# Optimization experiments

Measured on AMD Instinct MI355X. Metric: run time of the kernel, lower is better.

The kernel has to match this reference:

```python
import jax, jax.numpy as jnp
import numpy as np

NUM_HEADS = 8
DIM_HEAD = 128
SCALE = DIM_HEAD ** -0.5


def setup_inputs() -> dict:
    key = jax.random.key(0)
    ks = jax.random.split(key, 6)
    B, N, D = 8, 1024, 1024
    return {
        "s_v": jax.random.normal(ks[0], (B, N, D), jnp.float32),
        "s_m": jax.random.normal(ks[1], (B, N, D), jnp.float32),
        "g_l": jax.random.normal(ks[2], (B, NUM_HEADS, N, N), jnp.float32),
        "W_qkv": jax.random.normal(ks[3], (D, 3 * NUM_HEADS * DIM_HEAD), jnp.float32) * (D ** -0.5),
        "W_qk": jax.random.normal(ks[4], (D, 2 * NUM_HEADS * DIM_HEAD), jnp.float32) * (D ** -0.5),
        "W_out": jax.random.normal(ks[5], (NUM_HEADS * DIM_HEAD, D), jnp.float32) * ((NUM_HEADS * DIM_HEAD) ** -0.5),
        "b_out": jnp.zeros((D,), jnp.float32),
    }


def _split_heads(t):
    # [b, n, h*d] -> [b, h, n, d]
    b, n, hd = t.shape
    return t.reshape(b, n, NUM_HEADS, DIM_HEAD).transpose(0, 2, 1, 3)


def reference(s_v, s_m, g_l, W_qkv, W_qk, W_out, b_out):
    b, n, _ = s_v.shape
    q_v, k_v, v = [_split_heads(t) for t in jnp.split(s_v @ W_qkv, 3, axis=-1)]
    q_m, k_m = [_split_heads(t) for t in jnp.split(s_m @ W_qk, 2, axis=-1)]
    # trajectory attention probs (softmaxed) times raw value-stream scores
    p_m = jax.nn.softmax(jnp.einsum('bhid,bhjd->bhij', q_m, k_m), axis=-1)
    p_v = jnp.einsum('bhid,bhjd->bhij', q_v, k_v)
    dots = p_m * p_v * SCALE + g_l
    attn = jax.nn.softmax(dots, axis=-1)
    out = jnp.einsum('bhij,bhjd->bhid', attn, v)
    out = out.transpose(0, 2, 1, 3).reshape(b, n, NUM_HEADS * DIM_HEAD)
    return out @ W_out + b_out
```

## Files before the change

kernel.cpp:

```cpp
#include <hip/hip_runtime.h>

typedef __attribute__((ext_vector_type(8))) short short8;
typedef __attribute__((ext_vector_type(8))) unsigned short ushortx8;
typedef __attribute__((ext_vector_type(4))) unsigned short ushortx4;
typedef __attribute__((ext_vector_type(4))) float floatx4;

#define SCALE_F 0.08838834764831845f

__device__ __forceinline__ float b2f(unsigned short u) {
  union { unsigned int u; float f; } c; c.u = ((unsigned int)u) << 16; return c.f;
}
__device__ __forceinline__ unsigned short f2b(float f) {
  union { float f; unsigned int u; } c; c.f = f;
  unsigned int u = c.u;
  u += 0x7fffu + ((u >> 16) & 1u);
  return (unsigned short)(u >> 16);
}

#define GLD_LDS16(g, l)                                              \
  __builtin_amdgcn_global_load_lds(                                  \
      (const __attribute__((address_space(1))) void*)(g),            \
      (__attribute__((address_space(3))) void*)(l), 16, 0, 0)

__global__ __launch_bounds__(256) void cast_bf16_kernel(
    const float* __restrict__ x, unsigned short* __restrict__ y, int n) {
  int i = (blockIdx.x * 256 + threadIdx.x) * 4;
  if (i >= n) return;
  float4 v = *(const float4*)(x + i);
  ushortx4 o;
  o[0] = f2b(v.x); o[1] = f2b(v.y); o[2] = f2b(v.z); o[3] = f2b(v.w);
  *(ushortx4*)(y + i) = o;
}

__global__ __launch_bounds__(256) void split2_kernel(
    const float* __restrict__ x, unsigned short* __restrict__ y) {
  int idx = blockIdx.x * 256 + threadIdx.x;
  int row = idx >> 8;
  int c4 = (idx & 255) * 4;
  float4 v = *(const float4*)(x + (size_t)row * 1024 + c4);
  ushortx4 hi, lo;
  hi[0] = f2b(v.x); lo[0] = f2b(v.x - b2f(hi[0]));
  hi[1] = f2b(v.y); lo[1] = f2b(v.y - b2f(hi[1]));
  hi[2] = f2b(v.z); lo[2] = f2b(v.z - b2f(hi[2]));
  hi[3] = f2b(v.w); lo[3] = f2b(v.w - b2f(hi[3]));
  unsigned short* yr = y + (size_t)row * 2048;
  *(ushortx4*)(yr + c4) = hi;
  *(ushortx4*)(yr + 1024 + c4) = lo;
}

__global__ __launch_bounds__(256) void transpose_split_qk(
    const float* __restrict__ W, unsigned short* __restrict__ y) {
  __shared__ float tile[32][33];
  int t = threadIdx.x, tx = t & 31, ty = t >> 5;
  int n0 = blockIdx.x * 32, k0 = blockIdx.y * 32;
  for (int rr = ty; rr < 32; rr += 8)
    tile[rr][tx] = W[(size_t)(k0 + rr) * 2048 + n0 + tx];
  __syncthreads();
  for (int rr = ty; rr < 32; rr += 8) {
    float v = tile[tx][rr];
    unsigned short hi = f2b(v);
    unsigned short* yr = y + (size_t)(n0 + rr) * 2048;
    yr[k0 + tx] = hi;
    yr[1024 + k0 + tx] = hi;
  }
}

template<int MODE>
__global__ __launch_bounds__(256) void transpose_any(
    const void* __restrict__ inv, void* __restrict__ outv,
    int R, int C, int ldin, int ldout,
    long sIb, long sIh, long sOb, long sOh, int pstart) {
  int z = blockIdx.z, p = pstart + z, b = p >> 3, h = p & 7;
  size_t ioff = (size_t)(sIb * b + sIh * h);
  size_t ooff = (size_t)(sOb * b + sOh * h);
  __shared__ float tile[32][33];
  int t = threadIdx.x, tx = t & 31, ty = t >> 5;
  int c0 = blockIdx.x * 32, r0 = blockIdx.y * 32;
  for (int rr = ty; rr < 32; rr += 8) {
    size_t idx = ioff + (size_t)(r0 + rr) * ldin + (c0 + tx);
    tile[rr][tx] = (MODE == 2) ? b2f(((const unsigned short*)inv)[idx])
                               : ((const float*)inv)[idx];
  }
  __syncthreads();
  for (int rr = ty; rr < 32; rr += 8) {
    size_t idx = ooff + (size_t)(c0 + rr) * ldout + (r0 + tx);
    ((unsigned short*)outv)[idx] = f2b(tile[tx][rr]);
  }
}

template<int OUT_BF16, int ADD_BIAS>
__global__ __launch_bounds__(256) void gemm128(
    const unsigned short* __restrict__ A, const unsigned short* __restrict__ BT,
    void* __restrict__ Cv, const float* __restrict__ bias,
    int K, int lda, int ldb, int ldc,
    long sAz, long sAb, long sAh, long sBz, long sBb, long sBh,
    long sCz, long sCb, long sCh, int pstart) {
  int z = blockIdx.z, p = pstart + z, bb = p >> 3, hh = p & 7;
  A  += (size_t)(sAz * z + sAb * bb + sAh * hh);
  BT += (size_t)(sBz * z + sBb * bb + sBh * hh);
  size_t coff = (size_t)(sCz * z + sCb * bb + sCh * hh);

  __shared__ unsigned short Al[128][32];
  __shared__ unsigned short Bl[128][32];
  int t = threadIdx.x;
  int m0 = blockIdx.y * 128, n0 = blockIdx.x * 128;
  int w = t >> 6, l = t & 63;
  int wm = (w >> 1) * 64, wn = (w & 1) * 64;
  int lrow = l & 15, lq = l >> 4;
  floatx4 acc[4][4] = {};

  int srow = t >> 2, scol = (t & 3) * 8;
  const unsigned short* ga = A + (size_t)(m0 + srow) * lda + scol;
  const unsigned short* gb = BT + (size_t)(n0 + srow) * ldb + scol;
  unsigned short* la = &Al[srow][scol];
  unsigned short* lb = &Bl[srow][scol];
  size_t lda64 = (size_t)64 * lda, ldb64 = (size_t)64 * ldb;

  for (int k0 = 0; k0 < K; k0 += 32) {
    GLD_LDS16(ga + k0, la);
    GLD_LDS16(ga + lda64 + k0, la + 64 * 32);
    GLD_LDS16(gb + k0, lb);
    GLD_LDS16(gb + ldb64 + k0, lb + 64 * 32);
    __syncthreads();
    short8 af[4], bf[4];
#pragma unroll
    for (int i = 0; i < 4; i++) af[i] = *(const short8*)&Al[wm + i * 16 + lrow][lq * 8];
#pragma unroll
    for (int j = 0; j < 4; j++) bf[j] = *(const short8*)&Bl[wn + j * 16 + lrow][lq * 8];
#pragma unroll
    for (int i = 0; i < 4; i++)
#pragma unroll
      for (int j = 0; j < 4; j++)
        acc[i][j] = __builtin_amdgcn_mfma_f32_16x16x32_bf16(af[i], bf[j], acc[i][j], 0, 0, 0);
    __syncthreads();
  }
#pragma unroll
  for (int i = 0; i < 4; i++)
#pragma unroll
    for (int j = 0; j < 4; j++)
#pragma unroll
      for (int r = 0; r < 4; r++) {
        int row = m0 + wm + i * 16 + lq * 4 + r;
        int col = n0 + wn + j * 16 + lrow;
        float v = acc[i][j][r];
        if (ADD_BIAS) v += bias[col];
        size_t idx = coff + (size_t)row * ldc + col;
        if (OUT_BF16) ((unsigned short*)Cv)[idx] = f2b(v);
        else          ((float*)Cv)[idx] = v;
      }
}

template<int OUT_BF16, int ADD_BIAS>
__global__ __launch_bounds__(256) void gemm64(
    const unsigned short* __restrict__ A, const unsigned short* __restrict__ BT,
    void* __restrict__ Cv, const float* __restrict__ bias,
    int K, int lda, int ldb, int ldc,
    long sAz, long sAb, long sAh, long sBz, long sBb, long sBh,
    long sCz, long sCb, long sCh, int pstart) {
  int z = blockIdx.z, p = pstart + z, bb = p >> 3, hh = p & 7;
  A  += (size_t)(sAz * z + sAb * bb + sAh * hh);
  BT += (size_t)(sBz * z + sBb * bb + sBh * hh);
  size_t coff = (size_t)(sCz * z + sCb * bb + sCh * hh);

  __shared__ unsigned short Al[64][32];
  __shared__ unsigned short Bl[128][32];
  int t = threadIdx.x;
  int m0 = blockIdx.y * 64, n0 = blockIdx.x * 128;
  int w = t >> 6, l = t & 63;
  int wm = (w >> 1) * 32, wn = (w & 1) * 64;
  int lrow = l & 15, lq = l >> 4;
  floatx4 acc[2][4] = {};

  int srow = t >> 2, scol = (t & 3) * 8;
  const unsigned short* ga = A + (size_t)(m0 + srow) * lda + scol;
  const unsigned short* gb = BT + (size_t)(n0 + srow) * ldb + scol;
  unsigned short* la = &Al[srow][scol];
  unsigned short* lb = &Bl[srow][scol];
  size_t ldb64 = (size_t)64 * ldb;

  for (int k0 = 0; k0 < K; k0 += 32) {
    GLD_LDS16(ga + k0, la);
    GLD_LDS16(gb + k0, lb);
    GLD_LDS16(gb + ldb64 + k0, lb + 64 * 32);
    __syncthreads();
    short8 af[2], bf[4];
#pragma unroll
    for (int i = 0; i < 2; i++) af[i] = *(const short8*)&Al[wm + i * 16 + lrow][lq * 8];
#pragma unroll
    for (int j = 0; j < 4; j++) bf[j] = *(const short8*)&Bl[wn + j * 16 + lrow][lq * 8];
#pragma unroll
    for (int i = 0; i < 2; i++)
#pragma unroll
      for (int j = 0; j < 4; j++)
        acc[i][j] = __builtin_amdgcn_mfma_f32_16x16x32_bf16(af[i], bf[j], acc[i][j], 0, 0, 0);
    __syncthreads();
  }
#pragma unroll
  for (int i = 0; i < 2; i++)
#pragma unroll
    for (int j = 0; j < 4; j++)
#pragma unroll
      for (int r = 0; r < 4; r++) {
        int row = m0 + wm + i * 16 + lq * 4 + r;
        int col = n0 + wn + j * 16 + lrow;
        float v = acc[i][j][r];
        if (ADD_BIAS) v += bias[col];
        size_t idx = coff + (size_t)row * ldc + col;
        if (OUT_BF16) ((unsigned short*)Cv)[idx] = f2b(v);
        else          ((float*)Cv)[idx] = v;
      }
}

__global__ __launch_bounds__(256) void logits_prep(
    const float* __restrict__ qkf, unsigned short* __restrict__ qm,
    unsigned short* __restrict__ km, int pstart) {
  int idx = blockIdx.x * 256 + threadIdx.x;
  int z = blockIdx.y;
  int i = idx >> 5;
  int d4 = (idx & 31) * 4;
  int p = pstart + z, b = p >> 3, h = p & 7;
  const float* row = qkf + ((size_t)(b * 1024 + i)) * 2048 + h * 128;
  ushortx4 hi, lo;

  float4 q = *(const float4*)(row + d4);
  hi[0] = f2b(q.x); lo[0] = f2b(q.x - b2f(hi[0]));
  hi[1] = f2b(q.y); lo[1] = f2b(q.y - b2f(hi[1]));
  hi[2] = f2b(q.z); lo[2] = f2b(q.z - b2f(hi[2]));
  hi[3] = f2b(q.w); lo[3] = f2b(q.w - b2f(hi[3]));
  unsigned short* qr = qm + ((size_t)z * 1024 + i) * 384;
  *(ushortx4*)(qr + d4) = hi;
  *(ushortx4*)(qr + 128 + d4) = lo;
  *(ushortx4*)(qr + 256 + d4) = hi;

  float4 k = *(const float4*)(row + 1024 + d4);
  hi[0] = f2b(k.x); lo[0] = f2b(k.x - b2f(hi[0]));
  hi[1] = f2b(k.y); lo[1] = f2b(k.y - b2f(hi[1]));
  hi[2] = f2b(k.z); lo[2] = f2b(k.z - b2f(hi[2]));
  hi[3] = f2b(k.w); lo[3] = f2b(k.w - b2f(hi[3]));
  unsigned short* kr = km + ((size_t)z * 1024 + i) * 384;
  *(ushortx4*)(kr + d4) = hi;
  *(ushortx4*)(kr + 128 + d4) = hi;
  *(ushortx4*)(kr + 256 + d4) = lo;
}

__global__ __launch_bounds__(256) void softmax_combine(
    const float* __restrict__ smb, unsigned short* __restrict__ pvb,
    const float* __restrict__ g_l, int pstart) {
  int i = blockIdx.x, z = blockIdx.y;
  int p = pstart + z;
  const float* srow = smb + ((size_t)z * 1024 + i) * 1024;
  unsigned short* vrow = pvb + ((size_t)z * 1024 + i) * 1024;
  const float* grow = g_l + ((size_t)p * 1024 + i) * 1024;
  int t = threadIdx.x;
  __shared__ float red[4];

  float4 s = *(const float4*)(srow + t * 4);
  float mx = fmaxf(fmaxf(s.x, s.y), fmaxf(s.z, s.w));
#pragma unroll
  for (int o = 32; o; o >>= 1) mx = fmaxf(mx, __shfl_xor(mx, o));
  if ((t & 63) == 0) red[t >> 6] = mx;
  __syncthreads();
  mx = fmaxf(fmaxf(red[0], red[1]), fmaxf(red[2], red[3]));
  __syncthreads();
  float4 e;
  e.x = __expf(s.x - mx); e.y = __expf(s.y - mx);
  e.z = __expf(s.z - mx); e.w = __expf(s.w - mx);
  float sum = e.x + e.y + e.z + e.w;
#pragma unroll
  for (int o = 32; o; o >>= 1) sum += __shfl_xor(sum, o);
  if ((t & 63) == 0) red[t >> 6] = sum;
  __syncthreads();
  float inv = 1.0f / (red[0] + red[1] + red[2] + red[3]);
  __syncthreads();

  ushortx4 pv = *(const ushortx4*)(vrow + t * 4);
  float4 g = *(const float4*)(grow + t * 4);
  float4 d;
  d.x = e.x * inv * b2f(pv[0]) * SCALE_F + g.x;
  d.y = e.y * inv * b2f(pv[1]) * SCALE_F + g.y;
  d.z = e.z * inv * b2f(pv[2]) * SCALE_F + g.z;
  d.w = e.w * inv * b2f(pv[3]) * SCALE_F + g.w;

  float mx2 = fmaxf(fmaxf(d.x, d.y), fmaxf(d.z, d.w));
#pragma unroll
  for (int o = 32; o; o >>= 1) mx2 = fmaxf(mx2, __shfl_xor(mx2, o));
  if ((t & 63) == 0) red[t >> 6] = mx2;
  __syncthreads();
  mx2 = fmaxf(fmaxf(red[0], red[1]), fmaxf(red[2], red[3]));
  __syncthreads();
  float4 e2;
  e2.x = __expf(d.x - mx2); e2.y = __expf(d.y - mx2);
  e2.z = __expf(d.z - mx2); e2.w = __expf(d.w - mx2);
  float sum2 = e2.x + e2.y + e2.z + e2.w;
#pragma unroll
  for (int o = 32; o; o >>= 1) sum2 += __shfl_xor(sum2, o);
  if ((t & 63) == 0) red[t >> 6] = sum2;
  __syncthreads();
  float inv2 = 1.0f / (red[0] + red[1] + red[2] + red[3]);

  ushortx4 o4;
  o4[0] = f2b(e2.x * inv2); o4[1] = f2b(e2.y * inv2);
  o4[2] = f2b(e2.z * inv2); o4[3] = f2b(e2.w * inv2);
  *(ushortx4*)(vrow + t * 4) = o4;
}

extern "C" void kernel_launch(void* const* d_in, const int* in_sizes, int n_in,
                              void* d_out, int out_size, void* d_ws, size_t ws_size,
                              hipStream_t stream) {
  (void)in_sizes; (void)n_in; (void)out_size; (void)ws_size;
  const float* s_v   = (const float*)d_in[0];
  const float* s_m   = (const float*)d_in[1];
  const float* g_l   = (const float*)d_in[2];
  const float* W_qkv = (const float*)d_in[3];
  const float* W_qk  = (const float*)d_in[4];
  const float* W_out = (const float*)d_in[5];
  const float* b_out = (const float*)d_in[6];
  float* out = (float*)d_out;
  char* ws = (char*)d_ws;

  unsigned short* sv_bf  = (unsigned short*)(ws);
  unsigned short* qm384  = (unsigned short*)(ws);
  unsigned short* wtqkv  = (unsigned short*)(ws + 16777216);
  unsigned short* km384  = (unsigned short*)(ws + 16777216);
  unsigned short* wtout  = (unsigned short*)(ws + 29360128);
  unsigned short* qkvb   = (unsigned short*)(ws + 31457280);
  float*          qkf    = (float*)(ws + 81788928);
  unsigned short* vt     = (unsigned short*)(ws + 148897792);
  unsigned short* ao     = (unsigned short*)(ws + 165675008);
  unsigned short* smhl   = (unsigned short*)(ws + 182452224);
  float*          smb    = (float*)(ws + 182452224);
  unsigned short* wqk_hl = (unsigned short*)(ws + 249561088);
  unsigned short* pvb    = (unsigned short*)(ws + 249561088);

  cast_bf16_kernel<<<dim3(8192), 256, 0, stream>>>(s_v, sv_bf, 8388608);
  transpose_any<0><<<dim3(96, 32, 1), 256, 0, stream>>>(
      W_qkv, wtqkv, 1024, 3072, 3072, 1024, 0, 0, 0, 0, 0);
  transpose_any<0><<<dim3(32, 32, 1), 256, 0, stream>>>(
      W_out, wtout, 1024, 1024, 1024, 1024, 0, 0, 0, 0, 0);
  split2_kernel<<<dim3(8192), 256, 0, stream>>>(s_m, smhl);
  transpose_split_qk<<<dim3(64, 32, 1), 256, 0, stream>>>(W_qk, wqk_hl);
  gemm128<1, 0><<<dim3(24, 64, 1), 256, 0, stream>>>(
      sv_bf, wtqkv, qkvb, nullptr, 1024, 1024, 1024, 3072,
      0, 0, 0, 0, 0, 0, 0, 0, 0, 0);
  gemm128<0, 0><<<dim3(16, 64, 1), 256, 0, stream>>>(
      smhl, wqk_hl, qkf, nullptr, 2048, 2048, 2048, 2048,
      0, 0, 0, 0, 0, 0, 0, 0, 0, 0);
  transpose_any<2><<<dim3(4, 32, 64), 256, 0, stream>>>(
      qkvb + 2048, vt, 1024, 128, 3072, 1024,
      (long)1024 * 3072, 128, (long)1048576, 131072, 0);

  for (int c = 0; c < 4; c++) {
    int pstart = c * 16;
    logits_prep<<<dim3(128, 16), 256, 0, stream>>>(qkf, qm384, km384, pstart);
    gemm128<0, 0><<<dim3(8, 8, 16), 256, 0, stream>>>(
        qm384, km384, smb, nullptr, 384, 384, 384, 1024,
        (long)1024 * 384, 0, 0, (long)1024 * 384, 0, 0,
        (long)1048576, 0, 0, pstart);
    gemm128<1, 0><<<dim3(8, 8, 16), 256, 0, stream>>>(
        qkvb, qkvb + 1024, pvb, nullptr, 128, 3072, 3072, 1024,
        0, (long)1024 * 3072, 128, 0, (long)1024 * 3072, 128,
        (long)1048576, 0, 0, pstart);
    softmax_combine<<<dim3(1024, 16), 256, 0, stream>>>(smb, pvb, g_l, pstart);
    gemm64<1, 0><<<dim3(1, 16, 16), 256, 0, stream>>>(
        pvb, vt, ao, nullptr, 1024, 1024, 1024, 1024,
        (long)1048576, 0, 0, 0, (long)1048576, 131072,
        0, (long)1048576, 128, pstart);
  }
  gemm128<0, 1><<<dim3(8, 64, 1), 256, 0, stream>>>(
      ao, wtout, out, b_out, 1024, 1024, 1024, 1024,
      0, 0, 0, 0, 0, 0, 0, 0, 0, 0);
}
```

Measured before the change: 1.058 ms.

## Use wave-per-row softmax and single-pass batched attention when workspace allows

The softmax_combine kernel now gives each 64-lane wave one full row of 1024 elements. Reductions use only wave shuffles, with no shared memory or block barriers. When the workspace is large enough, a new memory layout holds all 64 batch-head slices at once, so the 4-chunk loop becomes one launch per stage, and the final attention-times-V GEMM switches from gemm64 to gemm128. This removes launch overhead and raises parallelism per launch, but needs a much larger workspace and falls back to the old chunked path if the workspace is too small.

```diff
diff --git a/kernel.cpp b/kernel.cpp
--- a/kernel.cpp
+++ b/kernel.cpp
@@ -246,68 +246,73 @@
 __global__ __launch_bounds__(256) void softmax_combine(
     const float* __restrict__ smb, unsigned short* __restrict__ pvb,
     const float* __restrict__ g_l, int pstart) {
-  int i = blockIdx.x, z = blockIdx.y;
-  int p = pstart + z;
+  int z = blockIdx.y, p = pstart + z;
+  int w = threadIdx.x >> 6, l = threadIdx.x & 63;
+  int i = blockIdx.x * 4 + w;
   const float* srow = smb + ((size_t)z * 1024 + i) * 1024;
   unsigned short* vrow = pvb + ((size_t)z * 1024 + i) * 1024;
   const float* grow = g_l + ((size_t)p * 1024 + i) * 1024;
-  int t = threadIdx.x;
-  __shared__ float red[4];
-
-  float4 s = *(const float4*)(srow + t * 4);
-  float mx = fmaxf(fmaxf(s.x, s.y), fmaxf(s.z, s.w));
+
+  float4 s[4];
+#pragma unroll
+  for (int j = 0; j < 4; j++) s[j] = *(const float4*)(srow + j * 256 + l * 4);
+  float mx = -3.0e38f;
+#pragma unroll
+  for (int j = 0; j < 4; j++)
+    mx = fmaxf(mx, fmaxf(fmaxf(s[j].x, s[j].y), fmaxf(s[j].z, s[j].w)));
 #pragma unroll
   for (int o = 32; o; o >>= 1) mx = fmaxf(mx, __shfl_xor(mx, o));
-  if ((t & 63) == 0) red[t >> 6] = mx;
-  __syncthreads();
-  mx = fmaxf(fmaxf(red[0], red[1]), fmaxf(red[2], red[3]));
-  __syncthreads();
-  float4 e;
-  e.x = __expf(s.x - mx); e.y = __expf(s.y - mx);
-  e.z = __expf(s.z - mx); e.w = __expf(s.w - mx);
-  float sum = e.x + e.y + e.z + e.w;
+  float sum = 0.0f;
+#pragma unroll
+  for (int j = 0; j < 4; j++) {
+    s[j].x = __expf(s[j].x - mx); s[j].y = __expf(s[j].y - mx);
+    s[j].z = __expf(s[j].z - mx); s[j].w = __expf(s[j].w - mx);
+    sum += (s[j].x + s[j].y) + (s[j].z + s[j].w);
+  }
 #pragma unroll
   for (int o = 32; o; o >>= 1) sum += __shfl_xor(sum, o);
-  if ((t & 63) == 0) red[t >> 6] = sum;
-  __syncthreads();
-  float inv = 1.0f / (red[0] + red[1] + red[2] + red[3]);
-  __syncthreads();
-
-  ushortx4 pv = *(const ushortx4*)(vrow + t * 4);
-  float4 g = *(const float4*)(grow + t * 4);
-  float4 d;
-  d.x = e.x * inv * b2f(pv[0]) * SCALE_F + g.x;
-  d.y = e.y * inv * b2f(pv[1]) * SCALE_F + g.y;
-  d.z = e.z * inv * b2f(pv[2]) * SCALE_F + g.z;
-  d.w = e.w * inv * b2f(pv[3]) * SCALE_F + g.w;
-
-  float mx2 = fmaxf(fmaxf(d.x, d.y), fmaxf(d.z, d.w));
+  float inv = 1.0f / sum;
+
+  float4 d[4];
+#pragma unroll
+  for (int j = 0; j < 4; j++) {
+    ushortx4 pv = *(const ushortx4*)(vrow + j * 256 + l * 4);
+    float4 g = *(const float4*)(grow + j * 256 + l * 4);
+    d[j].x = s[j].x * inv * b2f(pv[0]) * SCALE_F + g.x;
+    d[j].y = s[j].y * inv * b2f(pv[1]) * SCALE_F + g.y;
+    d[j].z = s[j].z * inv * b2f(pv[2]) * SCALE_F + g.z;
+    d[j].w = s[j].w * inv * b2f(pv[3]) * SCALE_F + g.w;
+  }
+  float mx2 = -3.0e38f;
+#pragma unroll
+  for (int j = 0; j < 4; j++)
+    mx2 = fmaxf(mx2, fmaxf(fmaxf(d[j].x, d[j].y), fmaxf(d[j].z, d[j].w)));
 #pragma unroll
   for (int o = 32; o; o >>= 1) mx2 = fmaxf(mx2, __shfl_xor(mx2, o));
-  if ((t & 63) == 0) red[t >> 6] = mx2;
-  __syncthreads();
-  mx2 = fmaxf(fmaxf(red[0], red[1]), fmaxf(red[2], red[3]));
-  __syncthreads();
-  float4 e2;
-  e2.x = __expf(d.x - mx2); e2.y = __expf(d.y - mx2);
-  e2.z = __expf(d.z - mx2); e2.w = __expf(d.w - mx2);
-  float sum2 = e2.x + e2.y + e2.z + e2.w;
+  float sum2 = 0.0f;
+#pragma unroll
+  for (int j = 0; j < 4; j++) {
+    d[j].x = __expf(d[j].x - mx2); d[j].y = __expf(d[j].y - mx2);
+    d[j].z = __expf(d[j].z - mx2); d[j].w = __expf(d[j].w - mx2);
+    sum2 += (d[j].x + d[j].y) + (d[j].z + d[j].w);
+  }
 #pragma unroll
   for (int o = 32; o; o >>= 1) sum2 += __shfl_xor(sum2, o);
-  if ((t & 63) == 0) red[t >> 6] = sum2;
-  __syncthreads();
-  float inv2 = 1.0f / (red[0] + red[1] + red[2] + red[3]);
-
-  ushortx4 o4;
-  o4[0] = f2b(e2.x * inv2); o4[1] = f2b(e2.y * inv2);
-  o4[2] = f2b(e2.z * inv2); o4[3] = f2b(e2.w * inv2);
-  *(ushortx4*)(vrow + t * 4) = o4;
+  float inv2 = 1.0f / sum2;
+
+#pragma unroll
+  for (int j = 0; j < 4; j++) {
+    ushortx4 o4;
+    o4[0] = f2b(d[j].x * inv2); o4[1] = f2b(d[j].y * inv2);
+    o4[2] = f2b(d[j].z * inv2); o4[3] = f2b(d[j].w * inv2);
+    *(ushortx4*)(vrow + j * 256 + l * 4) = o4;
+  }
 }
 
 extern "C" void kernel_launch(void* const* d_in, const int* in_sizes, int n_in,
                               void* d_out, int out_size, void* d_ws, size_t ws_size,
                               hipStream_t stream) {
-  (void)in_sizes; (void)n_in; (void)out_size; (void)ws_size;
+  (void)in_sizes; (void)n_in; (void)out_size;
   const float* s_v   = (const float*)d_in[0];
   const float* s_m   = (const float*)d_in[1];
   const float* g_l   = (const float*)d_in[2];
@@ -318,19 +323,40 @@
   float* out = (float*)d_out;
   char* ws = (char*)d_ws;
 
-  unsigned short* sv_bf  = (unsigned short*)(ws);
-  unsigned short* qm384  = (unsigned short*)(ws);
-  unsigned short* wtqkv  = (unsigned short*)(ws + 16777216);
-  unsigned short* km384  = (unsigned short*)(ws + 16777216);
-  unsigned short* wtout  = (unsigned short*)(ws + 29360128);
-  unsigned short* qkvb   = (unsigned short*)(ws + 31457280);
-  float*          qkf    = (float*)(ws + 81788928);
-  unsigned short* vt     = (unsigned short*)(ws + 148897792);
-  unsigned short* ao     = (unsigned short*)(ws + 165675008);
-  unsigned short* smhl   = (unsigned short*)(ws + 182452224);
-  float*          smb    = (float*)(ws + 182452224);
-  unsigned short* wqk_hl = (unsigned short*)(ws + 249561088);
-  unsigned short* pvb    = (unsigned short*)(ws + 249561088);
+  const bool big = (ws_size >= (size_t)721420288ull);
+
+  unsigned short *sv_bf, *qm384, *km384, *wtqkv, *wtout, *qkvb, *vt, *ao,
+                 *smhl, *wqk_hl, *pvb;
+  float *qkf, *smb;
+  if (big) {
+    sv_bf  = (unsigned short*)(ws);
+    wtqkv  = (unsigned short*)(ws + 16777216);
+    wtout  = (unsigned short*)(ws + 23068672);
+    qkvb   = (unsigned short*)(ws + 25165824);
+    qkf    = (float*)         (ws + 75497472);
+    vt     = (unsigned short*)(ws + 142606336);
+    ao     = (unsigned short*)(ws + 159383552);
+    smhl   = (unsigned short*)(ws + 176160768);
+    wqk_hl = (unsigned short*)(ws + 209715200);
+    qm384  = (unsigned short*)(ws + 218103808);
+    km384  = (unsigned short*)(ws + 268435456);
+    smb    = (float*)         (ws + 318767104);
+    pvb    = (unsigned short*)(ws + 587202560);
+  } else {
+    sv_bf  = (unsigned short*)(ws);
+    qm384  = (unsigned short*)(ws);
+    wtqkv  = (unsigned short*)(ws + 16777216);
+    km384  = (unsigned short*)(ws + 16777216);
+    wtout  = (unsigned short*)(ws + 29360128);
+    qkvb   = (unsigned short*)(ws + 31457280);
+    qkf    = (float*)         (ws + 81788928);
+    vt     = (unsigned short*)(ws + 148897792);
+    ao     = (unsigned short*)(ws + 165675008);
+    smhl   = (unsigned short*)(ws + 182452224);
+    smb    = (float*)         (ws + 182452224);
+    wqk_hl = (unsigned short*)(ws + 249561088);
+    pvb    = (unsigned short*)(ws + 249561088);
+  }
 
   cast_bf16_kernel<<<dim3(8192), 256, 0, stream>>>(s_v, sv_bf, 8388608);
   transpose_any<0><<<dim3(96, 32, 1), 256, 0, stream>>>(
@@ -349,22 +375,39 @@
       qkvb + 2048, vt, 1024, 128, 3072, 1024,
       (long)1024 * 3072, 128, (long)1048576, 131072, 0);
 
-  for (int c = 0; c < 4; c++) {
-    int pstart = c * 16;
-    logits_prep<<<dim3(128, 16), 256, 0, stream>>>(qkf, qm384, km384, pstart);
-    gemm128<0, 0><<<dim3(8, 8, 16), 256, 0, stream>>>(
+  if (big) {
+    logits_prep<<<dim3(128, 64), 256, 0, stream>>>(qkf, qm384, km384, 0);
+    gemm128<0, 0><<<dim3(8, 8, 64), 256, 0, stream>>>(
         qm384, km384, smb, nullptr, 384, 384, 384, 1024,
         (long)1024 * 384, 0, 0, (long)1024 * 384, 0, 0,
-        (long)1048576, 0, 0, pstart);
-    gemm128<1, 0><<<dim3(8, 8, 16), 256, 0, stream>>>(
+        (long)1048576, 0, 0, 0);
+    gemm128<1, 0><<<dim3(8, 8, 64), 256, 0, stream>>>(
         qkvb, qkvb + 1024, pvb, nullptr, 128, 3072, 3072, 1024,
         0, (long)1024 * 3072, 128, 0, (long)1024 * 3072, 128,
-        (long)1048576, 0, 0, pstart);
-    softmax_combine<<<dim3(1024, 16), 256, 0, stream>>>(smb, pvb, g_l, pstart);
-    gemm64<1, 0><<<dim3(1, 16, 16), 256, 0, stream>>>(
+        (long)1048576, 0, 0, 0);
+    softmax_combine<<<dim3(256, 64), 256, 0, stream>>>(smb, pvb, g_l, 0);
+    gemm128<1, 0><<<dim3(1, 8, 64), 256, 0, stream>>>(
         pvb, vt, ao, nullptr, 1024, 1024, 1024, 1024,
         (long)1048576, 0, 0, 0, (long)1048576, 131072,
-        0, (long)1048576, 128, pstart);
+        0, (long)1048576, 128, 0);
+  } else {
+    for (int c = 0; c < 4; c++) {
+      int pstart = c * 16;
+      logits_prep<<<dim3(128, 16), 256, 0, stream>>>(qkf, qm384, km384, pstart);
+      gemm128<0, 0><<<dim3(8, 8, 16), 256, 0, stream>>>(
+          qm384, km384, smb, nullptr, 384, 384, 384, 1024,
+          (long)1024 * 384, 0, 0, (long)1024 * 384, 0, 0,
+          (long)1048576, 0, 0, pstart);
+      gemm128<1, 0><<<dim3(8, 8, 16), 256, 0, stream>>>(
+          qkvb, qkvb + 1024, pvb, nullptr, 128, 3072, 3072, 1024,
+          0, (long)1024 * 3072, 128, 0, (long)1024 * 3072, 128,
+          (long)1048576, 0, 0, pstart);
+      softmax_combine<<<dim3(256, 16), 256, 0, stream>>>(smb, pvb, g_l, pstart);
+      gemm64<1, 0><<<dim3(1, 16, 16), 256, 0, stream>>>(
+          pvb, vt, ao, nullptr, 1024, 1024, 1024, 1024,
+          (long)1048576, 0, 0, 0, (long)1048576, 131072,
+          0, (long)1048576, 128, pstart);
+    }
   }
   gemm128<0, 1><<<dim3(8, 64, 1), 256, 0, stream>>>(
       ao, wtout, out, b_out, 1024, 1024, 1024, 1024,
```

After: 1.018 ms. -3.8%, faster.
